# Optimization experiments

Hardware: AMD Instinct MI355X
Metric: run time of the kernel (lower is better)

## Reference

```python
import jax, jax.numpy as jnp
import numpy as np


def _segsum(x):
    """Stable segment-sum. x: (..., l) -> (..., l, l) lower-triangular sums."""
    l = x.shape[-1]
    cs = jnp.cumsum(x, axis=-1)
    seg = cs[..., :, None] - cs[..., None, :]
    mask = jnp.tril(jnp.ones((l, l), dtype=bool))
    return jnp.where(mask, seg, -jnp.inf)


def setup_inputs() -> dict:
    key = jax.random.key(0)
    kx, ka, kb, kc = jax.random.split(key, 4)
    b, s, h, p, n = 4, 8192, 32, 64, 16
    X = jax.random.normal(kx, (b, s, h, p), dtype=jnp.float32)
    # negative A for realistic decaying SSM dynamics / numerical safety
    A = -jnp.abs(jax.random.normal(ka, (b, s, h), dtype=jnp.float32)) * 0.5
    B = jax.random.normal(kb, (b, s, h, n), dtype=jnp.float32)
    C = jax.random.normal(kc, (b, s, h, n), dtype=jnp.float32)
    return {"X": X, "A": A, "B": B, "C": C, "block_len": 64}


def reference(X, A, B, C, block_len):
    b, s, h, p = X.shape
    n = B.shape[-1]
    c = s // block_len
    l = block_len
    # chunk: (b, c, l, ...)
    Xb = X.reshape(b, c, l, h, p)
    Bb = B.reshape(b, c, l, h, n)
    Cb = C.reshape(b, c, l, h, n)
    Ab = A.reshape(b, c, l, h).transpose(0, 3, 1, 2)  # (b, h, c, l)
    A_cumsum = jnp.cumsum(Ab, axis=-1)                # (b, h, c, l)

    # 1) intra-chunk (diagonal) output
    L = jnp.exp(_segsum(Ab))                          # (b, h, c, l, l)
    Y_diag = jnp.einsum("bclhn,bcshn,bhcls,bcshp->bclhp", Cb, Bb, L, Xb)

    # 2) intra-chunk states (chunk-final state contribution)
    decay_states = jnp.exp(A_cumsum[..., -1:] - A_cumsum)   # (b, h, c, l)
    states = jnp.einsum("bclhn,bhcl,bclhp->bchpn", Bb, decay_states, Xb)

    # 3) inter-chunk recurrence (zero initial states)
    A_last = A_cumsum[..., -1]                        # (b, h, c)
    decay_chunk = jnp.exp(_segsum(jnp.pad(A_last, ((0, 0), (0, 0), (1, 0)))))  # (b,h,c+1,c+1)
    states = jnp.concatenate([jnp.zeros_like(states[:, :1]), states], axis=1)  # (b,c+1,h,p,n)
    new_states = jnp.einsum("bhzc,bchpn->bzhpn", decay_chunk, states)
    states = new_states[:, :-1]                       # states entering each chunk

    # 4) state -> output (off-diagonal)
    state_decay_out = jnp.exp(A_cumsum)               # (b, h, c, l)
    Y_off = jnp.einsum("bclhn,bchpn,bhcl->bclhp", Cb, states, state_decay_out)

    Y = (Y_diag + Y_off).reshape(b, s, h, p)
    return Y
```

## Files before the change

kernel.cpp:

```cpp
#include <hip/hip_runtime.h>

#define BB 4
#define SS 8192
#define HH 32
#define PP 64
#define NN 16
#define LL 64
#define CC 128

typedef __attribute__((ext_vector_type(8))) short bf16x8;
typedef __attribute__((ext_vector_type(4))) short bf16x4;
typedef __attribute__((ext_vector_type(4))) float f32x4;

__device__ inline short f2bf(float f) {
    unsigned u = __builtin_bit_cast(unsigned, f);
    u = (u + 0x7FFFu + ((u >> 16) & 1u)) >> 16;
    return (short)u;
}

__global__ __launch_bounds__(256) void k1_states(
    const float* __restrict__ X, const float* __restrict__ A,
    const float* __restrict__ B, float* __restrict__ states,
    float* __restrict__ a_last)
{
    int blk = blockIdx.x;
    int h = blk & (HH - 1);
    int c = (blk / HH) & (CC - 1);
    int b = blk / (HH * CC);
    int tid = threadIdx.x;

    __shared__ float Xs[LL][PP];
    __shared__ float Bs[LL][NN];
    __shared__ float cs[LL];

    const size_t row0 = (size_t)b * SS + (size_t)c * LL;
    const float* Xp = X + (row0 * HH + h) * PP;
    const float* Bp = B + (row0 * HH + h) * NN;
    const float* Ap = A + row0 * HH + h;

#pragma unroll
    for (int k = 0; k < 16; ++k) {
        int e = tid + k * 256;
        Xs[e >> 6][e & 63] = Xp[(size_t)(e >> 6) * (HH * PP) + (e & 63)];
    }
#pragma unroll
    for (int k = 0; k < 4; ++k) {
        int e = tid + k * 256;
        Bs[e >> 4][e & 15] = Bp[(size_t)(e >> 4) * (HH * NN) + (e & 15)];
    }
    if (tid < 64) {
        float x = Ap[(size_t)tid * HH];
#pragma unroll
        for (int d = 1; d < 64; d <<= 1) {
            float t = __shfl_up(x, d, 64);
            if (tid >= d) x += t;
        }
        cs[tid] = x;
    }
    __syncthreads();
    float alast = cs[LL - 1];
#pragma unroll
    for (int k = 0; k < 16; ++k) {
        int e = tid + k * 256;
        int r = e >> 6;
        Xs[r][e & 63] *= __expf(alast - cs[r]);
    }
    __syncthreads();

    int p  = tid >> 2;
    int nb = (tid & 3) << 2;
    float4 acc = {0.f, 0.f, 0.f, 0.f};
    for (int l = 0; l < LL; ++l) {
        float xv = Xs[l][p];
        const float4 bv = *(const float4*)&Bs[l][nb];
        acc.x += xv * bv.x; acc.y += xv * bv.y;
        acc.z += xv * bv.z; acc.w += xv * bv.w;
    }
    size_t bh = (size_t)b * HH + h;
    float* sp = states + ((bh * CC + c) * PP + p) * NN + nb;
    *(float4*)sp = acc;
    if (tid == 0) a_last[bh * CC + c] = alast;
}

__global__ __launch_bounds__(256) void k2_scan(
    float* __restrict__ states, const float* __restrict__ a_last)
{
    int idx = blockIdx.x * 256 + threadIdx.x;
    int pn = idx & (PP * NN - 1);
    int bh = idx >> 10;
    float* base = states + (size_t)bh * CC * (PP * NN) + pn;
    const float* al = a_last + (size_t)bh * CC;
    float carry = 0.f;
    for (int c0 = 0; c0 < CC; c0 += 8) {
        float s[8], av[8], o[8];
#pragma unroll
        for (int u = 0; u < 8; ++u) s[u] = base[(size_t)(c0 + u) * (PP * NN)];
#pragma unroll
        for (int u = 0; u < 8; ++u) av[u] = al[c0 + u];
#pragma unroll
        for (int u = 0; u < 8; ++u) { o[u] = carry; carry = __expf(av[u]) * carry + s[u]; }
#pragma unroll
        for (int u = 0; u < 8; ++u) base[(size_t)(c0 + u) * (PP * NN)] = o[u];
    }
}

__global__ __launch_bounds__(256) void k3_y(
    const float* __restrict__ X, const float* __restrict__ A,
    const float* __restrict__ Bm, const float* __restrict__ Cm,
    const float* __restrict__ Pst, float* __restrict__ Y)
{
    int blk = blockIdx.x;
    int h = blk & (HH - 1);
    int c = (blk / HH) & (CC - 1);
    int b = blk / (HH * CC);
    int tid = threadIdx.x;
    int w = tid >> 6, l = tid & 63, g = l >> 4, lr = l & 15;

    __shared__ short ScF[8 * 64 * 8];
    __shared__ short XTF[8 * 64 * 8];
    __shared__ short CsF[4 * 64 * 8];
    __shared__ short BsF[4 * 64 * 8];
    __shared__ short PsF[4 * 64 * 8];
    __shared__ float csL[64];

    const size_t row0 = (size_t)b * SS + (size_t)c * LL;
    const float* Xp = X + (row0 * HH + h) * PP;
    const float* Bp = Bm + (row0 * HH + h) * NN;
    const float* Cp = Cm + (row0 * HH + h) * NN;
    const float* Ap = A + row0 * HH + h;
    size_t bh = (size_t)b * HH + h;
    const float* Pp = Pst + (bh * CC + c) * (PP * NN);
    float* Yp = Y + (row0 * HH + h) * PP;

    ((bf16x8*)ScF)[tid] = (bf16x8)0;
    ((bf16x8*)ScF)[tid + 256] = (bf16x8)0;

    if (tid < 64) {
        float x = Ap[(size_t)tid * HH];
#pragma unroll
        for (int d = 1; d < 64; d <<= 1) {
            float t = __shfl_up(x, d, 64);
            if (tid >= d) x += t;
        }
        csL[tid] = x;
    }

    {
        int r = tid >> 2, q = tid & 3;
        int fl = (r & 15) + 16 * (q >> 1);
        int jt = r >> 4;
        float4 bv = *(const float4*)(Bp + (size_t)r * (HH * NN) + q * 4);
        float4 cv = *(const float4*)(Cp + (size_t)r * (HH * NN) + q * 4);
        float4 pv = *(const float4*)(Pp + tid * 4);
        bf16x4 bb = { f2bf(bv.x), f2bf(bv.y), f2bf(bv.z), f2bf(bv.w) };
        bf16x4 cc = { f2bf(cv.x), f2bf(cv.y), f2bf(cv.z), f2bf(cv.w) };
        bf16x4 pp = { f2bf(pv.x), f2bf(pv.y), f2bf(pv.z), f2bf(pv.w) };
        ((bf16x4*)BsF)[(jt * 64 + fl) * 2 + (q & 1)] = bb;
        ((bf16x4*)CsF)[(jt * 64 + fl) * 2 + (q & 1)] = cc;
        ((bf16x4*)PsF)[(jt * 64 + fl) * 2 + (q & 1)] = pp;
        int zt = tid >> 6, zu = (tid >> 1) & 31, zv = tid & 1;
        bf16x4 z = (bf16x4)0;
        ((bf16x4*)BsF)[(zt * 64 + 32 + zu) * 2 + zv] = z;
        ((bf16x4*)CsF)[(zt * 64 + 32 + zu) * 2 + zv] = z;
        ((bf16x4*)PsF)[(zt * 64 + 32 + zu) * 2 + zv] = z;
    }

#pragma unroll
    for (int si = 0; si < 2; ++si) {
        int s = tid + si * 256;
        int sl = s & 63, pt = (s >> 6) & 3, kt = s >> 8;
        int p = pt * 16 + (sl & 15);
        int k0 = kt * 32 + (sl >> 4) * 8;
        float xv[8];
#pragma unroll
        for (int e = 0; e < 8; ++e)
            xv[e] = Xp[(size_t)(k0 + e) * (HH * PP) + p];
        bf16x8 xb;
#pragma unroll
        for (int e = 0; e < 8; ++e) xb[e] = f2bf(xv[e]);
        ((bf16x8*)XTF)[s] = xb;
    }

    __syncthreads();

    float cs_i[4];
    int ib = w * 16 + g * 4;
#pragma unroll
    for (int r = 0; r < 4; ++r) cs_i[r] = csL[ib + r];

    bf16x8 caw = ((bf16x8*)CsF)[w * 64 + l];

    for (int jt = 0; jt <= w; ++jt) {
        bf16x8 bw = ((bf16x8*)BsF)[jt * 64 + l];
        f32x4 sr = __builtin_amdgcn_mfma_f32_16x16x32_bf16(caw, bw, (f32x4)0.f, 0, 0, 0);
        int j = jt * 16 + lr;
        float csj = csL[j];
        int kt = j >> 5;
        int flb = 16 * ((j >> 3) & 3);
#pragma unroll
        for (int r = 0; r < 4; ++r) {
            int i15 = g * 4 + r;
            int i = w * 16 + i15;
            float v = (j <= i) ? sr[r] * __expf(cs_i[r] - csj) : 0.f;
            ScF[((w * 2 + kt) * 64 + i15 + flb) * 8 + (j & 7)] = f2bf(v);
        }
    }

    f32x4 acc[4];
#pragma unroll
    for (int pt = 0; pt < 4; ++pt) {
        bf16x8 pw = ((bf16x8*)PsF)[pt * 64 + l];
        acc[pt] = __builtin_amdgcn_mfma_f32_16x16x32_bf16(caw, pw, (f32x4)0.f, 0, 0, 0);
    }
    float ei[4];
#pragma unroll
    for (int r = 0; r < 4; ++r) ei[r] = __expf(cs_i[r]);
#pragma unroll
    for (int pt = 0; pt < 4; ++pt)
#pragma unroll
        for (int r = 0; r < 4; ++r) acc[pt][r] *= ei[r];

    int kts = (w >= 2) ? 2 : 1;
    for (int kt = 0; kt < kts; ++kt) {
        bf16x8 af = ((bf16x8*)ScF)[(w * 2 + kt) * 64 + l];
#pragma unroll
        for (int pt = 0; pt < 4; ++pt) {
            bf16x8 xf = ((bf16x8*)XTF)[(kt * 4 + pt) * 64 + l];
            acc[pt] = __builtin_amdgcn_mfma_f32_16x16x32_bf16(af, xf, acc[pt], 0, 0, 0);
        }
    }

#pragma unroll
    for (int pt = 0; pt < 4; ++pt)
#pragma unroll
        for (int r = 0; r < 4; ++r) {
            int i = w * 16 + g * 4 + r;
            Yp[(size_t)i * (HH * PP) + pt * 16 + lr] = acc[pt][r];
        }
}

extern "C" void kernel_launch(void* const* d_in, const int* in_sizes, int n_in,
                              void* d_out, int out_size, void* d_ws, size_t ws_size,
                              hipStream_t stream)
{
    const float* X = (const float*)d_in[0];
    const float* A = (const float*)d_in[1];
    const float* B = (const float*)d_in[2];
    const float* C = (const float*)d_in[3];
    float* Y = (float*)d_out;

    float* states = (float*)d_ws;
    float* a_last = states + (size_t)BB * HH * CC * PP * NN;

    dim3 blk(256);
    k1_states<<<dim3(BB * CC * HH), blk, 0, stream>>>(X, A, B, states, a_last);
    k2_scan<<<dim3((BB * HH * PP * NN) / 256), blk, 0, stream>>>(states, a_last);
    k3_y<<<dim3(BB * CC * HH), blk, 0, stream>>>(X, A, B, C, states, Y);
}
```

Measured before the change: 263.0 us.

## Segment chunks into groups of eight and recompute per-chunk states inside the output kernel

Each block now processes a segment of 8 consecutive chunks for one (batch, head) chain. The first kernel writes only one carry per segment, and the scan runs over 16 segments instead of 128 chunks. The output kernel rebuilds the running state chunk by chunk with an extra MFMA over X and the decay-weighted B. This removes the large per-chunk state buffer write and read, at the cost of 8x fewer blocks (2048) and serial per-segment work that may hurt occupancy and latency hiding.

New measurement: 342.1 us. +30.1%, slower.

```diff
diff --git a/kernel.cpp b/kernel.cpp
--- a/kernel.cpp
+++ b/kernel.cpp
@@ -7,9 +7,12 @@
 #define NN 16
 #define LL 64
 #define CC 128
+#define SEG 8
+#define NSEG (CC / SEG)
+#define NCHAIN (BB * HH)
+#define NSEGT (NCHAIN * NSEG)
 
 typedef __attribute__((ext_vector_type(8))) short bf16x8;
-typedef __attribute__((ext_vector_type(4))) short bf16x4;
 typedef __attribute__((ext_vector_type(4))) float f32x4;
 
 __device__ inline short f2bf(float f) {
@@ -18,225 +21,259 @@
     return (short)u;
 }
 
-__global__ __launch_bounds__(256) void k1_states(
+__global__ __launch_bounds__(256) void k1_carries(
     const float* __restrict__ X, const float* __restrict__ A,
-    const float* __restrict__ B, float* __restrict__ states,
-    float* __restrict__ a_last)
-{
-    int blk = blockIdx.x;
-    int h = blk & (HH - 1);
-    int c = (blk / HH) & (CC - 1);
-    int b = blk / (HH * CC);
+    const float* __restrict__ B, float* __restrict__ carry,
+    float* __restrict__ segd)
+{
+    int seg = blockIdx.x;
+    int chain = seg >> 4;
+    int kseg = seg & (NSEG - 1);
+    int h = chain & (HH - 1);
+    int b = chain >> 5;
     int tid = threadIdx.x;
 
     __shared__ float Xs[LL][PP];
     __shared__ float Bs[LL][NN];
-    __shared__ float cs[LL];
-
-    const size_t row0 = (size_t)b * SS + (size_t)c * LL;
-    const float* Xp = X + (row0 * HH + h) * PP;
-    const float* Bp = B + (row0 * HH + h) * NN;
-    const float* Ap = A + row0 * HH + h;
-
-#pragma unroll
-    for (int k = 0; k < 16; ++k) {
-        int e = tid + k * 256;
-        Xs[e >> 6][e & 63] = Xp[(size_t)(e >> 6) * (HH * PP) + (e & 63)];
+    __shared__ float csL[LL];
+    __shared__ float wl[LL];
+
+    int p = tid >> 2, nb = (tid & 3) << 2;
+    float P0 = 0.f, P1 = 0.f, P2 = 0.f, P3 = 0.f;
+    float asum = 0.f;
+
+    for (int cc = 0; cc < SEG; ++cc) {
+        int c = kseg * SEG + cc;
+        size_t row0 = (size_t)b * SS + (size_t)c * LL;
+        const float* Xp = X + (row0 * HH + h) * PP;
+        const float* Bp = B + (row0 * HH + h) * NN;
+        const float* Ap = A + row0 * HH + h;
+
+#pragma unroll
+        for (int kk = 0; kk < 16; ++kk) {
+            int e = tid + kk * 256;
+            Xs[e >> 6][e & 63] = Xp[(size_t)(e >> 6) * (HH * PP) + (e & 63)];
+        }
+#pragma unroll
+        for (int kk = 0; kk < 4; ++kk) {
+            int e = tid + kk * 256;
+            Bs[e >> 4][e & 15] = Bp[(size_t)(e >> 4) * (HH * NN) + (e & 15)];
+        }
+        if (tid < 64) {
+            float x = Ap[(size_t)tid * HH];
+#pragma unroll
+            for (int d = 1; d < 64; d <<= 1) {
+                float t = __shfl_up(x, d, 64);
+                if (tid >= d) x += t;
+            }
+            csL[tid] = x;
+            float alast = __shfl(x, 63, 64);
+            wl[tid] = __expf(alast - x);
+        }
+        __syncthreads();
+
+        float alast = csL[LL - 1];
+        float s0 = 0.f, s1 = 0.f, s2 = 0.f, s3 = 0.f;
+        for (int l = 0; l < LL; ++l) {
+            float xw = Xs[l][p] * wl[l];
+            const float4 bv = *(const float4*)&Bs[l][nb];
+            s0 += xw * bv.x; s1 += xw * bv.y;
+            s2 += xw * bv.z; s3 += xw * bv.w;
+        }
+        float ea = __expf(alast);
+        P0 = ea * P0 + s0; P1 = ea * P1 + s1;
+        P2 = ea * P2 + s2; P3 = ea * P3 + s3;
+        asum += alast;
+        __syncthreads();
     }
-#pragma unroll
-    for (int k = 0; k < 4; ++k) {
-        int e = tid + k * 256;
-        Bs[e >> 4][e & 15] = Bp[(size_t)(e >> 4) * (HH * NN) + (e & 15)];
-    }
-    if (tid < 64) {
-        float x = Ap[(size_t)tid * HH];
-#pragma unroll
-        for (int d = 1; d < 64; d <<= 1) {
-            float t = __shfl_up(x, d, 64);
-            if (tid >= d) x += t;
-        }
-        cs[tid] = x;
-    }
-    __syncthreads();
-    float alast = cs[LL - 1];
-#pragma unroll
-    for (int k = 0; k < 16; ++k) {
-        int e = tid + k * 256;
-        int r = e >> 6;
-        Xs[r][e & 63] *= __expf(alast - cs[r]);
-    }
-    __syncthreads();
-
-    int p  = tid >> 2;
-    int nb = (tid & 3) << 2;
-    float4 acc = {0.f, 0.f, 0.f, 0.f};
-    for (int l = 0; l < LL; ++l) {
-        float xv = Xs[l][p];
-        const float4 bv = *(const float4*)&Bs[l][nb];
-        acc.x += xv * bv.x; acc.y += xv * bv.y;
-        acc.z += xv * bv.z; acc.w += xv * bv.w;
-    }
-    size_t bh = (size_t)b * HH + h;
-    float* sp = states + ((bh * CC + c) * PP + p) * NN + nb;
-    *(float4*)sp = acc;
-    if (tid == 0) a_last[bh * CC + c] = alast;
+    float4 pv = {P0, P1, P2, P3};
+    *(float4*)(carry + (size_t)seg * (PP * NN) + tid * 4) = pv;
+    if (tid == 0) segd[seg] = asum;
 }
 
 __global__ __launch_bounds__(256) void k2_scan(
-    float* __restrict__ states, const float* __restrict__ a_last)
-{
-    int idx = blockIdx.x * 256 + threadIdx.x;
-    int pn = idx & (PP * NN - 1);
-    int bh = idx >> 10;
-    float* base = states + (size_t)bh * CC * (PP * NN) + pn;
-    const float* al = a_last + (size_t)bh * CC;
-    float carry = 0.f;
-    for (int c0 = 0; c0 < CC; c0 += 8) {
-        float s[8], av[8], o[8];
-#pragma unroll
-        for (int u = 0; u < 8; ++u) s[u] = base[(size_t)(c0 + u) * (PP * NN)];
-#pragma unroll
-        for (int u = 0; u < 8; ++u) av[u] = al[c0 + u];
-#pragma unroll
-        for (int u = 0; u < 8; ++u) { o[u] = carry; carry = __expf(av[u]) * carry + s[u]; }
-#pragma unroll
-        for (int u = 0; u < 8; ++u) base[(size_t)(c0 + u) * (PP * NN)] = o[u];
+    const float* __restrict__ carry, const float* __restrict__ segd,
+    float* __restrict__ pin)
+{
+    int chain = blockIdx.x >> 2;
+    int t = ((blockIdx.x & 3) << 8) + threadIdx.x;
+    const float* cb = carry + (size_t)chain * NSEG * (PP * NN) + t;
+    float* pb = pin + (size_t)chain * NSEG * (PP * NN) + t;
+    const float* as = segd + chain * NSEG;
+    float P = 0.f;
+    for (int kk = 0; kk < NSEG; ++kk) {
+        float s = cb[(size_t)kk * (PP * NN)];
+        pb[(size_t)kk * (PP * NN)] = P;
+        P = __expf(as[kk]) * P + s;
     }
 }
 
 __global__ __launch_bounds__(256) void k3_y(
     const float* __restrict__ X, const float* __restrict__ A,
     const float* __restrict__ Bm, const float* __restrict__ Cm,
-    const float* __restrict__ Pst, float* __restrict__ Y)
-{
-    int blk = blockIdx.x;
-    int h = blk & (HH - 1);
-    int c = (blk / HH) & (CC - 1);
-    int b = blk / (HH * CC);
+    const float* __restrict__ pin, float* __restrict__ Y)
+{
+    int seg = blockIdx.x;
+    int chain = seg >> 4;
+    int kseg = seg & (NSEG - 1);
+    int h = chain & (HH - 1);
+    int b = chain >> 5;
     int tid = threadIdx.x;
     int w = tid >> 6, l = tid & 63, g = l >> 4, lr = l & 15;
 
+    __shared__ short XTF[8 * 64 * 8];
     __shared__ short ScF[8 * 64 * 8];
-    __shared__ short XTF[8 * 64 * 8];
-    __shared__ short CsF[4 * 64 * 8];
-    __shared__ short BsF[4 * 64 * 8];
-    __shared__ short PsF[4 * 64 * 8];
-    __shared__ float csL[64];
-
-    const size_t row0 = (size_t)b * SS + (size_t)c * LL;
-    const float* Xp = X + (row0 * HH + h) * PP;
-    const float* Bp = Bm + (row0 * HH + h) * NN;
-    const float* Cp = Cm + (row0 * HH + h) * NN;
-    const float* Ap = A + row0 * HH + h;
-    size_t bh = (size_t)b * HH + h;
-    const float* Pp = Pst + (bh * CC + c) * (PP * NN);
-    float* Yp = Y + (row0 * HH + h) * PP;
+    __shared__ float Bp32[LL][17];
+    __shared__ short PT16[NN * 68];
+    __shared__ float csL[LL];
+    __shared__ float wl[LL];
 
     ((bf16x8*)ScF)[tid] = (bf16x8)0;
     ((bf16x8*)ScF)[tid + 256] = (bf16x8)0;
 
-    if (tid < 64) {
-        float x = Ap[(size_t)tid * HH];
-#pragma unroll
-        for (int d = 1; d < 64; d <<= 1) {
-            float t = __shfl_up(x, d, 64);
-            if (tid >= d) x += t;
-        }
-        csL[tid] = x;
+    float4 pv = *(const float4*)(pin + (size_t)seg * (PP * NN) + (16 * w + lr) * NN + 4 * g);
+    float P[4] = {pv.x, pv.y, pv.z, pv.w};
+
+    for (int cc = 0; cc < SEG; ++cc) {
+        int c = kseg * SEG + cc;
+        size_t row0 = (size_t)b * SS + (size_t)c * LL;
+        const float* Xp = X + (row0 * HH + h) * PP;
+        const float* Bp = Bm + (row0 * HH + h) * NN;
+        const float* Cp = Cm + (row0 * HH + h) * NN;
+        const float* Ap = A + row0 * HH + h;
+        float* Yp = Y + (row0 * HH + h) * PP;
+
+#pragma unroll
+        for (int r = 0; r < 4; ++r)
+            PT16[(4 * g + r) * 68 + 16 * w + lr] = f2bf(P[r]);
+
+        if (tid < 64) {
+            float x = Ap[(size_t)tid * HH];
+#pragma unroll
+            for (int d = 1; d < 64; d <<= 1) {
+                float t = __shfl_up(x, d, 64);
+                if (tid >= d) x += t;
+            }
+            csL[tid] = x;
+            float alast = __shfl(x, 63, 64);
+            wl[tid] = __expf(alast - x);
+        }
+#pragma unroll
+        for (int kk = 0; kk < 4; ++kk) {
+            int e = tid + kk * 256;
+            Bp32[e >> 4][e & 15] = Bp[(size_t)(e >> 4) * (HH * NN) + (e & 15)];
+        }
+#pragma unroll
+        for (int si = 0; si < 2; ++si) {
+            int s = tid + si * 256;
+            int sl = s & 63, pt = (s >> 6) & 3, kt = s >> 8;
+            int pp = pt * 16 + (sl & 15);
+            int k0 = kt * 32 + (sl >> 4) * 8;
+            bf16x8 xb;
+#pragma unroll
+            for (int e = 0; e < 8; ++e)
+                xb[e] = f2bf(Xp[(size_t)(k0 + e) * (HH * PP) + pp]);
+            ((bf16x8*)XTF)[s] = xb;
+        }
+        bf16x8 caw = (bf16x8)0;
+        if (g < 2) {
+            const float* cr = Cp + (size_t)(16 * w + lr) * (HH * NN) + g * 8;
+            float4 a0 = *(const float4*)cr;
+            float4 a1 = *(const float4*)(cr + 4);
+            caw[0] = f2bf(a0.x); caw[1] = f2bf(a0.y);
+            caw[2] = f2bf(a0.z); caw[3] = f2bf(a0.w);
+            caw[4] = f2bf(a1.x); caw[5] = f2bf(a1.y);
+            caw[6] = f2bf(a1.z); caw[7] = f2bf(a1.w);
+        }
+        __syncthreads();
+
+        float alast = csL[LL - 1];
+        float cs_i[4], ei[4];
+        int ib = 16 * w + 4 * g;
+#pragma unroll
+        for (int r = 0; r < 4; ++r) { cs_i[r] = csL[ib + r]; ei[r] = __expf(cs_i[r]); }
+
+        bf16x8 pf[4];
+#pragma unroll
+        for (int pt = 0; pt < 4; ++pt) {
+            bf16x8 t = (bf16x8)0;
+            if (g < 2) {
+#pragma unroll
+                for (int e = 0; e < 8; ++e)
+                    t[e] = PT16[(g * 8 + e) * 68 + pt * 16 + lr];
+            }
+            pf[pt] = t;
+        }
+        bf16x8 bt[2];
+#pragma unroll
+        for (int kt = 0; kt < 2; ++kt) {
+            bf16x8 t;
+#pragma unroll
+            for (int e = 0; e < 8; ++e) {
+                int ll = kt * 32 + g * 8 + e;
+                t[e] = f2bf(Bp32[ll][lr] * wl[ll]);
+            }
+            bt[kt] = t;
+        }
+
+        for (int jt = 0; jt <= w; ++jt) {
+            bf16x8 bw = (bf16x8)0;
+            if (g < 2) {
+#pragma unroll
+                for (int e = 0; e < 8; ++e)
+                    bw[e] = f2bf(Bp32[jt * 16 + lr][g * 8 + e]);
+            }
+            f32x4 sr = __builtin_amdgcn_mfma_f32_16x16x32_bf16(caw, bw, (f32x4)0.f, 0, 0, 0);
+            int j = jt * 16 + lr;
+            float csj = csL[j];
+            int kt2 = j >> 5;
+            int flb = 16 * ((j >> 3) & 3);
+#pragma unroll
+            for (int r = 0; r < 4; ++r) {
+                int i15 = g * 4 + r;
+                int i = 16 * w + i15;
+                float v = (j <= i) ? sr[r] * __expf(cs_i[r] - csj) : 0.f;
+                ScF[((w * 2 + kt2) * 64 + i15 + flb) * 8 + (j & 7)] = f2bf(v);
+            }
+        }
+
+        f32x4 acc[4];
+#pragma unroll
+        for (int pt = 0; pt < 4; ++pt)
+            acc[pt] = __builtin_amdgcn_mfma_f32_16x16x32_bf16(caw, pf[pt], (f32x4)0.f, 0, 0, 0);
+#pragma unroll
+        for (int pt = 0; pt < 4; ++pt)
+#pragma unroll
+            for (int r = 0; r < 4; ++r) acc[pt][r] *= ei[r];
+
+        int kts = (w >= 2) ? 2 : 1;
+        for (int kt = 0; kt < kts; ++kt) {
+            bf16x8 af = ((bf16x8*)ScF)[(w * 2 + kt) * 64 + l];
+#pragma unroll
+            for (int pt = 0; pt < 4; ++pt) {
+                bf16x8 xf = ((bf16x8*)XTF)[(kt * 4 + pt) * 64 + l];
+                acc[pt] = __builtin_amdgcn_mfma_f32_16x16x32_bf16(af, xf, acc[pt], 0, 0, 0);
+            }
+        }
+
+        f32x4 st = (f32x4)0.f;
+#pragma unroll
+        for (int kt = 0; kt < 2; ++kt) {
+            bf16x8 xf = ((bf16x8*)XTF)[(kt * 4 + w) * 64 + l];
+            st = __builtin_amdgcn_mfma_f32_16x16x32_bf16(bt[kt], xf, st, 0, 0, 0);
+        }
+        float ea = __expf(alast);
+#pragma unroll
+        for (int r = 0; r < 4; ++r) P[r] = ea * P[r] + st[r];
+
+#pragma unroll
+        for (int pt = 0; pt < 4; ++pt)
+#pragma unroll
+            for (int r = 0; r < 4; ++r)
+                Yp[(size_t)(16 * w + 4 * g + r) * (HH * PP) + pt * 16 + lr] = acc[pt][r];
+
+        __syncthreads();
     }
-
-    {
-        int r = tid >> 2, q = tid & 3;
-        int fl = (r & 15) + 16 * (q >> 1);
-        int jt = r >> 4;
-        float4 bv = *(const float4*)(Bp + (size_t)r * (HH * NN) + q * 4);
-        float4 cv = *(const float4*)(Cp + (size_t)r * (HH * NN) + q * 4);
-        float4 pv = *(const float4*)(Pp + tid * 4);
-        bf16x4 bb = { f2bf(bv.x), f2bf(bv.y), f2bf(bv.z), f2bf(bv.w) };
-        bf16x4 cc = { f2bf(cv.x), f2bf(cv.y), f2bf(cv.z), f2bf(cv.w) };
-        bf16x4 pp = { f2bf(pv.x), f2bf(pv.y), f2bf(pv.z), f2bf(pv.w) };
-        ((bf16x4*)BsF)[(jt * 64 + fl) * 2 + (q & 1)] = bb;
-        ((bf16x4*)CsF)[(jt * 64 + fl) * 2 + (q & 1)] = cc;
-        ((bf16x4*)PsF)[(jt * 64 + fl) * 2 + (q & 1)] = pp;
-        int zt = tid >> 6, zu = (tid >> 1) & 31, zv = tid & 1;
-        bf16x4 z = (bf16x4)0;
-        ((bf16x4*)BsF)[(zt * 64 + 32 + zu) * 2 + zv] = z;
-        ((bf16x4*)CsF)[(zt * 64 + 32 + zu) * 2 + zv] = z;
-        ((bf16x4*)PsF)[(zt * 64 + 32 + zu) * 2 + zv] = z;
-    }
-
-#pragma unroll
-    for (int si = 0; si < 2; ++si) {
-        int s = tid + si * 256;
-        int sl = s & 63, pt = (s >> 6) & 3, kt = s >> 8;
-        int p = pt * 16 + (sl & 15);
-        int k0 = kt * 32 + (sl >> 4) * 8;
-        float xv[8];
-#pragma unroll
-        for (int e = 0; e < 8; ++e)
-            xv[e] = Xp[(size_t)(k0 + e) * (HH * PP) + p];
-        bf16x8 xb;
-#pragma unroll
-        for (int e = 0; e < 8; ++e) xb[e] = f2bf(xv[e]);
-        ((bf16x8*)XTF)[s] = xb;
-    }
-
-    __syncthreads();
-
-    float cs_i[4];
-    int ib = w * 16 + g * 4;
-#pragma unroll
-    for (int r = 0; r < 4; ++r) cs_i[r] = csL[ib + r];
-
-    bf16x8 caw = ((bf16x8*)CsF)[w * 64 + l];
-
-    for (int jt = 0; jt <= w; ++jt) {
-        bf16x8 bw = ((bf16x8*)BsF)[jt * 64 + l];
-        f32x4 sr = __builtin_amdgcn_mfma_f32_16x16x32_bf16(caw, bw, (f32x4)0.f, 0, 0, 0);
-        int j = jt * 16 + lr;
-        float csj = csL[j];
-        int kt = j >> 5;
-        int flb = 16 * ((j >> 3) & 3);
-#pragma unroll
-        for (int r = 0; r < 4; ++r) {
-            int i15 = g * 4 + r;
-            int i = w * 16 + i15;
-            float v = (j <= i) ? sr[r] * __expf(cs_i[r] - csj) : 0.f;
-            ScF[((w * 2 + kt) * 64 + i15 + flb) * 8 + (j & 7)] = f2bf(v);
-        }
-    }
-
-    f32x4 acc[4];
-#pragma unroll
-    for (int pt = 0; pt < 4; ++pt) {
-        bf16x8 pw = ((bf16x8*)PsF)[pt * 64 + l];
-        acc[pt] = __builtin_amdgcn_mfma_f32_16x16x32_bf16(caw, pw, (f32x4)0.f, 0, 0, 0);
-    }
-    float ei[4];
-#pragma unroll
-    for (int r = 0; r < 4; ++r) ei[r] = __expf(cs_i[r]);
-#pragma unroll
-    for (int pt = 0; pt < 4; ++pt)
-#pragma unroll
-        for (int r = 0; r < 4; ++r) acc[pt][r] *= ei[r];
-
-    int kts = (w >= 2) ? 2 : 1;
-    for (int kt = 0; kt < kts; ++kt) {
-        bf16x8 af = ((bf16x8*)ScF)[(w * 2 + kt) * 64 + l];
-#pragma unroll
-        for (int pt = 0; pt < 4; ++pt) {
-            bf16x8 xf = ((bf16x8*)XTF)[(kt * 4 + pt) * 64 + l];
-            acc[pt] = __builtin_amdgcn_mfma_f32_16x16x32_bf16(af, xf, acc[pt], 0, 0, 0);
-        }
-    }
-
-#pragma unroll
-    for (int pt = 0; pt < 4; ++pt)
-#pragma unroll
-        for (int r = 0; r < 4; ++r) {
-            int i = w * 16 + g * 4 + r;
-            Yp[(size_t)i * (HH * PP) + pt * 16 + lr] = acc[pt][r];
-        }
 }
 
 extern "C" void kernel_launch(void* const* d_in, const int* in_sizes, int n_in,
@@ -249,11 +286,12 @@
     const float* C = (const float*)d_in[3];
     float* Y = (float*)d_out;
 
-    float* states = (float*)d_ws;
-    float* a_last = states + (size_t)BB * HH * CC * PP * NN;
+    float* carry = (float*)d_ws;
+    float* pin   = carry + (size_t)NSEGT * (PP * NN);
+    float* segd  = pin   + (size_t)NSEGT * (PP * NN);
 
     dim3 blk(256);
-    k1_states<<<dim3(BB * CC * HH), blk, 0, stream>>>(X, A, B, states, a_last);
-    k2_scan<<<dim3((BB * HH * PP * NN) / 256), blk, 0, stream>>>(states, a_last);
-    k3_y<<<dim3(BB * CC * HH), blk, 0, stream>>>(X, A, B, C, states, Y);
-}
+    k1_carries<<<dim3(NSEGT), blk, 0, stream>>>(X, A, B, carry, segd);
+    k2_scan<<<dim3(NCHAIN * 4), blk, 0, stream>>>(carry, segd, pin);
+    k3_y<<<dim3(NSEGT), blk, 0, stream>>>(X, A, B, C, pin, Y);
+}
```
